# Optimization experiments

Measured on AMD Instinct MI355X. Metric: run time of the kernel, lower is better.

## Reference

```python
import jax, jax.numpy as jnp
import numpy as np

GAMMA = 0.99
LMBD = 0.95  # lambda is unused in live math: in-loop advantages are overwritten by returns - values
EPS = 0.2
T, S, H, A = 262144, 128, 1024, 16


def setup_inputs() -> dict:
    key = jax.random.key(0)
    ks = jax.random.split(key, 12)
    states = jax.random.normal(ks[0], (T, S), jnp.float32)
    actions = jax.random.normal(ks[1], (T, A), jnp.float32)
    rewards = jax.random.normal(ks[2], (T, 1), jnp.float32)
    values = jax.random.normal(ks[3], (T, 1), jnp.float32)
    masks = jax.random.randint(ks[4], (T, 1), 0, 2, jnp.int32)
    W1 = jax.random.normal(ks[5], (S, H), jnp.float32) / np.sqrt(S)
    b1 = jnp.zeros((H,), jnp.float32)
    W_mu = jax.random.normal(ks[6], (H, A), jnp.float32) / np.sqrt(H)
    b_mu = jnp.zeros((A,), jnp.float32)
    W_lv = jax.random.normal(ks[7], (H, A), jnp.float32) / np.sqrt(H)
    b_lv = jnp.zeros((A,), jnp.float32)
    # beta (old policy) log-probs: computed from the same net + small noise so that
    # ratio = exp(sum(pi_logp - beta_logp)) stays numerically reasonable, as in real PPO.
    h = jnp.tanh(states @ W1 + b1)
    mu = h @ W_mu + b_mu
    std = jnp.exp(0.5 * (h @ W_lv + b_lv))
    logp = -0.5 * jnp.square((actions - mu) / std) - jnp.log(std) - 0.5 * jnp.log(2.0 * jnp.pi)
    beta_log_probs = logp + 0.01 * jax.random.normal(ks[8], (T, A), jnp.float32)
    return dict(states=states, actions=actions, rewards=rewards, values=values,
                beta_log_probs=beta_log_probs, W1=W1, b1=b1, W_mu=W_mu, b_mu=b_mu,
                W_lv=W_lv, b_lv=b_lv, masks=masks)


def reference(states, actions, rewards, values, beta_log_probs,
              W1, b1, W_mu, b_mu, W_lv, b_lv, masks):
    m = masks.astype(rewards.dtype)  # [T,1] 1=continue, 0=episode boundary

    # reversed masked discounted-return recurrence: returns[i] = r[i] + gamma * prev_return * m[i]
    def step(prev_ret, inp):
        r, mi = inp
        ret = r + GAMMA * prev_ret * mi
        return ret, ret

    _, returns = jax.lax.scan(step, jnp.zeros((1,), rewards.dtype), (rewards, m), reverse=True)
    # (deltas / in-loop GAE advantages in the source are dead code: overwritten below)
    advantages = returns - values                      # [T,1]
    a_hat = (advantages - advantages.mean()) / (advantages.std(ddof=1) + 1e-7)

    # pi(states) -> mu, logvar (value head unused here)
    h = jnp.tanh(states @ W1 + b1)                     # [T,H]
    mu = h @ W_mu + b_mu                               # [T,A]
    logvar = h @ W_lv + b_lv
    std = jnp.exp(0.5 * logvar)
    pi_log_probs = -0.5 * jnp.square((actions - mu) / std) - jnp.log(std) - 0.5 * jnp.log(2.0 * jnp.pi)

    blp = jax.lax.stop_gradient(beta_log_probs)        # .detach() in source
    ratio = jnp.exp(jnp.sum(pi_log_probs - blp, axis=1, keepdims=True))  # [T,1]

    actor_loss = -jnp.mean(jnp.minimum(ratio * a_hat,
                                       jnp.clip(ratio, 1.0 - EPS, 1.0 + EPS) * a_hat))
    critic_loss = jnp.mean(jnp.square(advantages))
    return actor_loss + critic_loss
```

## Files before the change

### kernel.cpp

```cpp
#include <hip/hip_runtime.h>
#include <math.h>


typedef __attribute__((ext_vector_type(8))) short short8_t;
typedef __attribute__((ext_vector_type(4))) short short4_t;
typedef __attribute__((ext_vector_type(4))) float float4_t;
typedef __attribute__((ext_vector_type(2))) unsigned uint2_t;
typedef __attribute__((ext_vector_type(4))) unsigned uint4_t;

#define T_TOTAL 262144
#define S_DIM 128
#define H_DIM 1024
#define A_DIM 16
#define GAMMA 0.99f
#define LOG2E2 2.8853900817779268f
#define SEG_LEN 64
#define NSEG 4096
#define GRP 16
#define NGRP 256

#define WS_SUM   0
#define WS_SUMSQ 1
#define WS_MEAN  2
#define WS_ISTD  3
#define WS_TERM  4
#define WS_SEGA  8
#define WS_SEGB  (WS_SEGA + NSEG)
#define WS_INC   (WS_SEGB + NSEG)
#define WS_SEGP  (WS_INC + NSEG)
#define WS_SEGQ  (WS_SEGP + NSEG)
#define WS_SEGR  (WS_SEGQ + NSEG)
#define WS_SEGS2 (WS_SEGR + NSEG)
#define WS_SEGT2 (WS_SEGS2 + NSEG)
#define WS_B1S   (WS_SEGT2 + NSEG)
#define WS_W1F   (WS_B1S + 1024)
#define WS_WHF   (WS_W1F + 65536)

#define SM_SIZE (16384 + 256 + 16)

__device__ __forceinline__ short f2bf(float f) {
  unsigned u = __float_as_uint(f);
  u += 0x7fffu + ((u >> 16) & 1u);
  return (short)(u >> 16);
}

__device__ __forceinline__ unsigned cvt_pk_bf16(float lo, float hi) {
  unsigned r;
  asm("v_cvt_pk_bf16_f32 %0, %1, %2" : "=v"(r) : "v"(lo), "v"(hi));
  return r;
}

__device__ __forceinline__ void permlane32_swap2(unsigned& a, unsigned& b) {
  asm("v_permlane32_swap_b32 %0, %1" : "+v"(a), "+v"(b));
}

__device__ __forceinline__ float tanh2(float x, float bs) {
  float a = __builtin_fmaf(x, LOG2E2, bs);
  float e = __builtin_amdgcn_exp2f(a);
  float r = __builtin_amdgcn_rcpf(e + 1.0f);
  return __builtin_fmaf(r, -2.0f, 1.0f);
}

__global__ void prep_all(const float* __restrict__ W1,
                         const float* __restrict__ W_mu,
                         const float* __restrict__ W_lv,
                         const float* __restrict__ b1,
                         const float* __restrict__ rewards,
                         const int* __restrict__ masks,
                         const float* __restrict__ values,
                         float* __restrict__ ws,
                         short* __restrict__ w1f,
                         short* __restrict__ whf) {
  const int blk = blockIdx.x;
  if (blk < 64) {
    int id = blk * 256 + threadIdx.x;
    int lane = id & 63;
    int kf = (id >> 6) & 3;
    int nt = id >> 8;
    int quad = lane >> 4, col = nt * 16 + (lane & 15);
    int kbase = kf * 32 + quad * 8;
#pragma unroll
    for (int e = 0; e < 8; ++e)
      w1f[(size_t)id * 8 + e] = f2bf(W1[(size_t)(kbase + e) * H_DIM + col]);
  } else if (blk < 80) {
    int id = (blk - 64) * 256 + threadIdx.x;
    int lane = id & 63;
    int kf = (id >> 6) & 31;
    int nt = id >> 11;
    const float* src = nt ? W_lv : W_mu;
    int quad = lane >> 4, col = lane & 15;
    int hbase = kf * 32 + ((quad >> 1) << 4) + ((quad & 1) << 2);
#pragma unroll
    for (int e = 0; e < 8; ++e) {
      int hh = hbase + ((e >> 2) << 3) + (e & 3);
      whf[(size_t)id * 8 + e] = f2bf(src[(size_t)hh * A_DIM + col]);
    }
  } else if (blk < 96) {
    int g = (blk - 80) * 256 + threadIdx.x;
    int lo = g * SEG_LEN;
    const float4* r4 = (const float4*)(rewards + lo);
    const int4* m4 = (const int4*)(masks + lo);
    const float4* v4 = (const float4*)(values + lo);
    float a = 1.0f, b = 0.0f;
    float P = 0.0f, Q = 0.0f, R = 0.0f, S2 = 0.0f, T2 = 0.0f;
#pragma unroll 4
    for (int c = 15; c >= 0; --c) {
      float4 r = r4[c]; int4 mm = m4[c]; float4 v = v4[c];
      float gi, d;
      gi = GAMMA * (float)mm.w; b = r.w + gi * b; a = gi * a;
      d = b - v.w; P += a; Q += d; R += a * d; S2 += d * d; T2 += a * a;
      gi = GAMMA * (float)mm.z; b = r.z + gi * b; a = gi * a;
      d = b - v.z; P += a; Q += d; R += a * d; S2 += d * d; T2 += a * a;
      gi = GAMMA * (float)mm.y; b = r.y + gi * b; a = gi * a;
      d = b - v.y; P += a; Q += d; R += a * d; S2 += d * d; T2 += a * a;
      gi = GAMMA * (float)mm.x; b = r.x + gi * b; a = gi * a;
      d = b - v.x; P += a; Q += d; R += a * d; S2 += d * d; T2 += a * a;
    }
    ws[WS_SEGA + g] = a;
    ws[WS_SEGB + g] = b;
    ws[WS_SEGP + g] = P;
    ws[WS_SEGQ + g] = Q;
    ws[WS_SEGR + g] = R;
    ws[WS_SEGS2 + g] = S2;
    ws[WS_SEGT2 + g] = T2;
  } else {
    if (threadIdx.x < 8) ws[threadIdx.x] = 0.0f;
    int base = threadIdx.x * 4;
    float4 bv = *(const float4*)(b1 + base);
    float4 o;
    o.x = LOG2E2 * bv.x; o.y = LOG2E2 * bv.y;
    o.z = LOG2E2 * bv.z; o.w = LOG2E2 * bv.w;
    *(float4*)(ws + WS_B1S + base) = o;
  }
}

__global__ void scan_pass2(float* __restrict__ ws) {
  __shared__ float gA[NGRP], gB[NGRP], ginc[NGRP];
  __shared__ float rs1[4], rs2[4];
  int t = threadIdx.x;
  int lo = t * GRP, hi = lo + GRP - 1;
  float A = 1.0f, B = 0.0f;
  for (int s = hi; s >= lo; --s) {
    float as = ws[WS_SEGA + s], bs = ws[WS_SEGB + s];
    B = bs + as * B;
    A = as * A;
  }
  gA[t] = A; gB[t] = B;
  __syncthreads();
  if (t == 0) {
    float x = 0.0f;
    ginc[NGRP - 1] = 0.0f;
    for (int g = NGRP - 1; g >= 1; --g) {
      x = gB[g] + gA[g] * x;
      ginc[g - 1] = x;
    }
  }
  __syncthreads();
  float x = ginc[t];
  float sum = 0.0f, sumsq = 0.0f;
  for (int s = hi; s >= lo; --s) {
    ws[WS_INC + s] = x;
    float P = ws[WS_SEGP + s], Q = ws[WS_SEGQ + s], R = ws[WS_SEGR + s];
    float S2 = ws[WS_SEGS2 + s], T2 = ws[WS_SEGT2 + s];
    sum += Q + P * x;
    sumsq += S2 + (2.0f * R + T2 * x) * x;
    x = ws[WS_SEGB + s] + ws[WS_SEGA + s] * x;
  }
  int lane = t & 63, wv = t >> 6;
#pragma unroll
  for (int m = 1; m < 64; m <<= 1) {
    sum += __shfl_xor(sum, m);
    sumsq += __shfl_xor(sumsq, m);
  }
  if (lane == 0) { rs1[wv] = sum; rs2[wv] = sumsq; }
  __syncthreads();
  if (t == 0) {
    float s1 = rs1[0] + rs1[1] + rs1[2] + rs1[3];
    float s2 = rs2[0] + rs2[1] + rs2[2] + rs2[3];
    float n = (float)T_TOTAL;
    ws[WS_SUM] = s1;
    ws[WS_SUMSQ] = s2;
    float mean = s1 / n;
    float var = (s2 - s1 * s1 / n) / (n - 1.0f);
    var = fmaxf(var, 0.0f);
    ws[WS_MEAN] = mean;
    ws[WS_ISTD] = 1.0f / (sqrtf(var) + 1e-7f);
  }
}

__launch_bounds__(256, 2)
__global__ void main2(const float* __restrict__ states,
                      const float* __restrict__ actions,
                      const float* __restrict__ beta,
                      const float* __restrict__ rewards,
                      const int* __restrict__ masks,
                      const float* __restrict__ values,
                      const float* __restrict__ b1s,
                      const float* __restrict__ bmug,
                      const float* __restrict__ blvg,
                      const short* __restrict__ W1f,
                      const short* __restrict__ Whf,
                      float* __restrict__ ws) {
  __shared__ __align__(16) unsigned char smem[SM_SIZE];
  short* Ab = (short*)smem;
  float* adv_lds = (float*)(smem + 16384);
  float* lds_term = (float*)(smem + 16384 + 256);

  const int tid = threadIdx.x;
  const int lane = tid & 63;
  const int w = tid >> 6;
  const int quad = lane >> 4;
  const int t0 = blockIdx.x * 64;

  if (w == 0) {
    float r = rewards[t0 + lane];
    float g = GAMMA * (float)masks[t0 + lane];
    float v = values[t0 + lane];
    float SA = g, SB = r;
#pragma unroll
    for (int off = 1; off < 64; off <<= 1) {
      float tA = __shfl_down(SA, off);
      float tB = __shfl_down(SB, off);
      if (lane + off < 64) { SB = SB + SA * tB; SA = SA * tA; }
    }
    float x = ws[WS_INC + blockIdx.x];
    adv_lds[lane] = (SB + SA * x) - v;
  }

  {
    const float4* src = (const float4*)(states + (size_t)t0 * S_DIM);
#pragma unroll
    for (int i = 0; i < 8; ++i) {
      int f = tid + i * 256;
      float4 v = src[f];
      int row = f >> 5, kq = f & 31;
      int rt = row >> 4, rr = row & 15;
      int k = kq * 4, kf = k >> 5, qd = (k >> 3) & 3, j0 = k & 7;
      uint2_t pk2;
      pk2[0] = cvt_pk_bf16(v.x, v.y);
      pk2[1] = cvt_pk_bf16(v.z, v.w);
      *(uint2_t*)(Ab + (((rt * 4 + kf) * 64 + qd * 16 + rr) << 3) + j0) = pk2;
    }
  }
  __syncthreads();

  short8_t sfrag[4][4];
#pragma unroll
  for (int rt = 0; rt < 4; ++rt)
#pragma unroll
    for (int kf = 0; kf < 4; ++kf)
      sfrag[rt][kf] = *((const short8_t*)Ab + (rt * 4 + kf) * 64 + lane);

  float4_t acc2[4][2];
#pragma unroll
  for (int rt = 0; rt < 4; ++rt) {
    acc2[rt][0] = (float4_t){0.f, 0.f, 0.f, 0.f};
    acc2[rt][1] = (float4_t){0.f, 0.f, 0.f, 0.f};
  }
  const float4_t zz = (float4_t){0.f, 0.f, 0.f, 0.f};

  for (int kk = 0; kk < 8; ++kk) {
    const int nt1 = w * 16 + kk * 2;
    const short8_t* w1p = (const short8_t*)W1f + nt1 * 256 + lane;
    short8_t wf0[4], wf1[4];
#pragma unroll
    for (int kf = 0; kf < 4; ++kf) {
      wf0[kf] = w1p[kf * 64];
      wf1[kf] = w1p[256 + kf * 64];
    }
    const float4 b1a = *(const float4*)(b1s + nt1 * 16 + quad * 4);
    const float4 b1b = *(const float4*)(b1s + nt1 * 16 + 16 + quad * 4);
    const int kf2 = w * 8 + kk;
    const short8_t* whp = (const short8_t*)Whf + kf2 * 64 + lane;
    const short8_t wmu = whp[0];
    const short8_t wlv = whp[2048];
#pragma unroll
    for (int rt = 0; rt < 4; ++rt) {
      float4_t c0 = zz;
      float4_t c1 = zz;
#pragma unroll
      for (int kf = 0; kf < 4; ++kf) {
        c0 = __builtin_amdgcn_mfma_f32_16x16x32_bf16(wf0[kf], sfrag[rt][kf], c0, 0, 0, 0);
        c1 = __builtin_amdgcn_mfma_f32_16x16x32_bf16(wf1[kf], sfrag[rt][kf], c1, 0, 0, 0);
      }
      unsigned p00 = cvt_pk_bf16(tanh2(c0[0], b1a.x), tanh2(c0[1], b1a.y));
      unsigned p01 = cvt_pk_bf16(tanh2(c0[2], b1a.z), tanh2(c0[3], b1a.w));
      unsigned p10 = cvt_pk_bf16(tanh2(c1[0], b1b.x), tanh2(c1[1], b1b.y));
      unsigned p11 = cvt_pk_bf16(tanh2(c1[2], b1b.z), tanh2(c1[3], b1b.w));
      permlane32_swap2(p00, p10);
      permlane32_swap2(p01, p11);
      uint4_t u = (uint4_t){p00, p01, p10, p11};
      short8_t b2 = __builtin_bit_cast(short8_t, u);
      acc2[rt][0] = __builtin_amdgcn_mfma_f32_16x16x32_bf16(wmu, b2, acc2[rt][0], 0, 0, 0);
      acc2[rt][1] = __builtin_amdgcn_mfma_f32_16x16x32_bf16(wlv, b2, acc2[rt][1], 0, 0, 0);
    }
  }

  __syncthreads();
  float* red = (float*)smem;
  if (w < 2) {
#pragma unroll
    for (int rt = 0; rt < 4; ++rt)
#pragma unroll
      for (int nt = 0; nt < 2; ++nt)
        *(float4_t*)(red + ((((w & 1) * 8 + rt * 2 + nt) * 64 + lane) << 2)) = acc2[rt][nt];
  }
  __syncthreads();
  if (w >= 2) {
#pragma unroll
    for (int rt = 0; rt < 4; ++rt)
#pragma unroll
      for (int nt = 0; nt < 2; ++nt) {
        float* p = red + ((((w & 1) * 8 + rt * 2 + nt) * 64 + lane) << 2);
        float4_t v = *(float4_t*)p;
        v += acc2[rt][nt];
        *(float4_t*)p = v;
      }
  }
  __syncthreads();

  const float mean = ws[WS_MEAN], istd = ws[WS_ISTD];

  const int rt = w;
  const int tcol = lane & 15;
  const int t = t0 + rt * 16 + tcol;
  const float4 bmu4 = *(const float4*)(bmug + quad * 4);
  const float4 blv4 = *(const float4*)(blvg + quad * 4);
  float m0 = bmu4.x, m1 = bmu4.y, m2 = bmu4.z, m3 = bmu4.w;
  float l0 = blv4.x, l1 = blv4.y, l2 = blv4.z, l3 = blv4.w;
  const float4_t* rp = (const float4_t*)red;
#pragma unroll
  for (int r = 0; r < 2; ++r) {
    float4_t mv = rp[(r * 8 + rt * 2 + 0) * 64 + lane];
    float4_t lvv = rp[(r * 8 + rt * 2 + 1) * 64 + lane];
    m0 += mv[0]; m1 += mv[1]; m2 += mv[2]; m3 += mv[3];
    l0 += lvv[0]; l1 += lvv[1]; l2 += lvv[2]; l3 += lvv[3];
  }
  const float4 av = *(const float4*)(actions + (size_t)t * A_DIM + quad * 4);
  const float4 bv = *(const float4*)(beta + (size_t)t * A_DIM + quad * 4);
  float d = 0.0f;
  {
    float isd, z;
    isd = __expf(-0.5f * l0); z = (av.x - m0) * isd;
    d += -0.5f * z * z - 0.5f * l0 - 0.9189385332046727f - bv.x;
    isd = __expf(-0.5f * l1); z = (av.y - m1) * isd;
    d += -0.5f * z * z - 0.5f * l1 - 0.9189385332046727f - bv.y;
    isd = __expf(-0.5f * l2); z = (av.z - m2) * isd;
    d += -0.5f * z * z - 0.5f * l2 - 0.9189385332046727f - bv.z;
    isd = __expf(-0.5f * l3); z = (av.w - m3) * isd;
    d += -0.5f * z * z - 0.5f * l3 - 0.9189385332046727f - bv.w;
  }
  d += __shfl_xor(d, 16);
  d += __shfl_xor(d, 32);
  float term = 0.0f;
  if (quad == 0) {
    float ratio = __expf(d);
    float ah = (adv_lds[rt * 16 + tcol] - mean) * istd;
    float rc = fminf(fmaxf(ratio, 0.8f), 1.2f);
    term = fminf(ratio * ah, rc * ah);
  }
  term += __shfl_xor(term, 1);
  term += __shfl_xor(term, 2);
  term += __shfl_xor(term, 4);
  term += __shfl_xor(term, 8);
  if (lane == 0) lds_term[w] = term;
  __syncthreads();
  if (tid == 0)
    atomicAdd(&ws[WS_TERM], lds_term[0] + lds_term[1] + lds_term[2] + lds_term[3]);
}

__global__ void finalize(const float* __restrict__ ws, float* __restrict__ out) {
  if (threadIdx.x == 0) {
    float n = (float)T_TOTAL;
    out[0] = ws[WS_SUMSQ] / n - ws[WS_TERM] / n;
  }
}

extern "C" void kernel_launch(void* const* d_in, const int* in_sizes, int n_in,
                              void* d_out, int out_size, void* d_ws, size_t ws_size,
                              hipStream_t stream) {
  const float* states  = (const float*)d_in[0];
  const float* actions = (const float*)d_in[1];
  const float* rewards = (const float*)d_in[2];
  const float* values  = (const float*)d_in[3];
  const float* beta    = (const float*)d_in[4];
  const float* W1      = (const float*)d_in[5];
  const float* b1      = (const float*)d_in[6];
  const float* W_mu    = (const float*)d_in[7];
  const float* b_mu    = (const float*)d_in[8];
  const float* W_lv    = (const float*)d_in[9];
  const float* b_lv    = (const float*)d_in[10];
  const int*   masks   = (const int*)d_in[11];
  float* ws = (float*)d_ws;
  float* out = (float*)d_out;
  short* w1f = (short*)(ws + WS_W1F);
  short* whf = (short*)(ws + WS_WHF);
  const float* b1s = ws + WS_B1S;

  hipLaunchKernelGGL(prep_all, dim3(97), dim3(256), 0, stream,
                     W1, W_mu, W_lv, b1, rewards, masks, values, ws, w1f, whf);
  hipLaunchKernelGGL(scan_pass2, dim3(1), dim3(NGRP), 0, stream, ws);
  hipLaunchKernelGGL(main2, dim3(T_TOTAL / 64), dim3(256), 0, stream,
                     states, actions, beta, rewards, masks, values,
                     b1s, b_mu, b_lv, w1f, whf, ws);
  hipLaunchKernelGGL(finalize, dim3(1), dim3(64), 0, stream, ws, out);
}
```

Measured before the change: 327.2 us.

## Fold global return scan into main kernel via claimed block and flag wait

Removes the separate single-block scan kernel. The first block of the main kernel to win an atomic claim now runs the cross-segment return scan and the advantage mean/std reduction, then publishes the results with a release flag. Every block does its matmul work first and spin-waits on that flag only before it needs the mean, inv-std and segment carry-in, so the serial scan overlaps with the GEMM work instead of sitting between launches. The launch-bounds occupancy hint also goes from 2 to 3 blocks, which may force fewer registers and cause spills. The claiming block is delayed by the serial scan, and correctness depends on the claim and flag words being reset by the preceding prep kernel.

```diff
diff --git a/kernel.cpp b/kernel.cpp
--- a/kernel.cpp
+++ b/kernel.cpp
@@ -24,6 +24,8 @@
 #define WS_MEAN  2
 #define WS_ISTD  3
 #define WS_TERM  4
+#define WS_FLAG  5
+#define WS_CLAIM 6
 #define WS_SEGA  8
 #define WS_SEGB  (WS_SEGA + NSEG)
 #define WS_INC   (WS_SEGB + NSEG)
@@ -36,7 +38,7 @@
 #define WS_W1F   (WS_B1S + 1024)
 #define WS_WHF   (WS_W1F + 65536)
 
-#define SM_SIZE (16384 + 256 + 16)
+#define SM_SIZE (16384 + 256 + 32)
 
 __device__ __forceinline__ short f2bf(float f) {
   unsigned u = __float_as_uint(f);
@@ -134,61 +136,7 @@
   }
 }
 
-__global__ void scan_pass2(float* __restrict__ ws) {
-  __shared__ float gA[NGRP], gB[NGRP], ginc[NGRP];
-  __shared__ float rs1[4], rs2[4];
-  int t = threadIdx.x;
-  int lo = t * GRP, hi = lo + GRP - 1;
-  float A = 1.0f, B = 0.0f;
-  for (int s = hi; s >= lo; --s) {
-    float as = ws[WS_SEGA + s], bs = ws[WS_SEGB + s];
-    B = bs + as * B;
-    A = as * A;
-  }
-  gA[t] = A; gB[t] = B;
-  __syncthreads();
-  if (t == 0) {
-    float x = 0.0f;
-    ginc[NGRP - 1] = 0.0f;
-    for (int g = NGRP - 1; g >= 1; --g) {
-      x = gB[g] + gA[g] * x;
-      ginc[g - 1] = x;
-    }
-  }
-  __syncthreads();
-  float x = ginc[t];
-  float sum = 0.0f, sumsq = 0.0f;
-  for (int s = hi; s >= lo; --s) {
-    ws[WS_INC + s] = x;
-    float P = ws[WS_SEGP + s], Q = ws[WS_SEGQ + s], R = ws[WS_SEGR + s];
-    float S2 = ws[WS_SEGS2 + s], T2 = ws[WS_SEGT2 + s];
-    sum += Q + P * x;
-    sumsq += S2 + (2.0f * R + T2 * x) * x;
-    x = ws[WS_SEGB + s] + ws[WS_SEGA + s] * x;
-  }
-  int lane = t & 63, wv = t >> 6;
-#pragma unroll
-  for (int m = 1; m < 64; m <<= 1) {
-    sum += __shfl_xor(sum, m);
-    sumsq += __shfl_xor(sumsq, m);
-  }
-  if (lane == 0) { rs1[wv] = sum; rs2[wv] = sumsq; }
-  __syncthreads();
-  if (t == 0) {
-    float s1 = rs1[0] + rs1[1] + rs1[2] + rs1[3];
-    float s2 = rs2[0] + rs2[1] + rs2[2] + rs2[3];
-    float n = (float)T_TOTAL;
-    ws[WS_SUM] = s1;
-    ws[WS_SUMSQ] = s2;
-    float mean = s1 / n;
-    float var = (s2 - s1 * s1 / n) / (n - 1.0f);
-    var = fmaxf(var, 0.0f);
-    ws[WS_MEAN] = mean;
-    ws[WS_ISTD] = 1.0f / (sqrtf(var) + 1e-7f);
-  }
-}
-
-__launch_bounds__(256, 2)
+__launch_bounds__(256, 3)
 __global__ void main2(const float* __restrict__ states,
                       const float* __restrict__ actions,
                       const float* __restrict__ beta,
@@ -212,19 +160,69 @@
   const int quad = lane >> 4;
   const int t0 = blockIdx.x * 64;
 
-  if (w == 0) {
-    float r = rewards[t0 + lane];
-    float g = GAMMA * (float)masks[t0 + lane];
-    float v = values[t0 + lane];
-    float SA = g, SB = r;
-#pragma unroll
-    for (int off = 1; off < 64; off <<= 1) {
-      float tA = __shfl_down(SA, off);
-      float tB = __shfl_down(SB, off);
-      if (lane + off < 64) { SB = SB + SA * tB; SA = SA * tA; }
-    }
-    float x = ws[WS_INC + blockIdx.x];
-    adv_lds[lane] = (SB + SA * x) - v;
+  if (tid == 0) {
+    unsigned old = atomicCAS((unsigned*)&ws[WS_CLAIM], 0u, 1u);
+    ((unsigned*)lds_term)[7] = (old == 0u) ? 1u : 0u;
+  }
+  __syncthreads();
+  if (((unsigned*)lds_term)[7]) {
+    float* gA = (float*)smem;
+    float* gB = gA + NGRP;
+    float* ginc = gB + NGRP;
+    float* rs = ginc + NGRP;
+    int t = tid;
+    int lo = t * GRP, hi = lo + GRP - 1;
+    float A = 1.0f, B = 0.0f;
+    for (int s = hi; s >= lo; --s) {
+      float as = ws[WS_SEGA + s], bs = ws[WS_SEGB + s];
+      B = bs + as * B;
+      A = as * A;
+    }
+    gA[t] = A; gB[t] = B;
+    __syncthreads();
+    if (t == 0) {
+      float x = 0.0f;
+      ginc[NGRP - 1] = 0.0f;
+      for (int g = NGRP - 1; g >= 1; --g) {
+        x = gB[g] + gA[g] * x;
+        ginc[g - 1] = x;
+      }
+    }
+    __syncthreads();
+    float x = ginc[t];
+    float sum = 0.0f, sumsq = 0.0f;
+    for (int s = hi; s >= lo; --s) {
+      atomicExch(&ws[WS_INC + s], x);
+      float P = ws[WS_SEGP + s], Q = ws[WS_SEGQ + s], R = ws[WS_SEGR + s];
+      float S2 = ws[WS_SEGS2 + s], T2 = ws[WS_SEGT2 + s];
+      sum += Q + P * x;
+      sumsq += S2 + (2.0f * R + T2 * x) * x;
+      x = ws[WS_SEGB + s] + ws[WS_SEGA + s] * x;
+    }
+    int ln = t & 63, wv = t >> 6;
+#pragma unroll
+    for (int m = 1; m < 64; m <<= 1) {
+      sum += __shfl_xor(sum, m);
+      sumsq += __shfl_xor(sumsq, m);
+    }
+    if (ln == 0) { rs[wv] = sum; rs[4 + wv] = sumsq; }
+    __syncthreads();
+    if (t == 0) {
+      float s1 = rs[0] + rs[1] + rs[2] + rs[3];
+      float s2 = rs[4] + rs[5] + rs[6] + rs[7];
+      float n = (float)T_TOTAL;
+      float mean = s1 / n;
+      float var = (s2 - s1 * s1 / n) / (n - 1.0f);
+      var = fmaxf(var, 0.0f);
+      atomicExch(&ws[WS_SUM], s1);
+      atomicExch(&ws[WS_SUMSQ], s2);
+      atomicExch(&ws[WS_MEAN], mean);
+      atomicExch(&ws[WS_ISTD], 1.0f / (sqrtf(var) + 1e-7f));
+      __threadfence();
+      __hip_atomic_store((unsigned*)&ws[WS_FLAG], 1u,
+                         __ATOMIC_RELEASE, __HIP_MEMORY_SCOPE_AGENT);
+    }
+    __syncthreads();
   }
 
   {
@@ -319,7 +317,33 @@
   }
   __syncthreads();
 
-  const float mean = ws[WS_MEAN], istd = ws[WS_ISTD];
+  if (tid == 0) {
+    while (__hip_atomic_load((unsigned*)&ws[WS_FLAG],
+                             __ATOMIC_ACQUIRE, __HIP_MEMORY_SCOPE_AGENT) == 0u) {
+      __builtin_amdgcn_s_sleep(1);
+    }
+    lds_term[4] = atomicAdd(&ws[WS_MEAN], 0.0f);
+    lds_term[5] = atomicAdd(&ws[WS_ISTD], 0.0f);
+    lds_term[6] = atomicAdd(&ws[WS_INC + blockIdx.x], 0.0f);
+  }
+  __syncthreads();
+
+  if (w == 0) {
+    float r = rewards[t0 + lane];
+    float g = GAMMA * (float)masks[t0 + lane];
+    float v = values[t0 + lane];
+    float SA = g, SB = r;
+#pragma unroll
+    for (int off = 1; off < 64; off <<= 1) {
+      float tA = __shfl_down(SA, off);
+      float tB = __shfl_down(SB, off);
+      if (lane + off < 64) { SB = SB + SA * tB; SA = SA * tA; }
+    }
+    adv_lds[lane] = (SB + SA * lds_term[6]) - v;
+  }
+  __syncthreads();
+
+  const float mean = lds_term[4], istd = lds_term[5];
 
   const int rt = w;
   const int tcol = lane & 15;
@@ -399,7 +423,6 @@
 
   hipLaunchKernelGGL(prep_all, dim3(97), dim3(256), 0, stream,
                      W1, W_mu, W_lv, b1, rewards, masks, values, ws, w1f, whf);
-  hipLaunchKernelGGL(scan_pass2, dim3(1), dim3(NGRP), 0, stream, ws);
   hipLaunchKernelGGL(main2, dim3(T_TOTAL / 64), dim3(256), 0, stream,
                      states, actions, beta, rewards, masks, values,
                      b1s, b_mu, b_lv, w1f, whf, ws);
```

Measured after the change: 715.5 us. 2.19x slower.
